# Kernel tuning notes

Hardware: AMD Instinct MI355X
Metric: run time of the kernel (lower is better)

The kernel has to match this reference:

```python
import jax, jax.numpy as jnp
import numpy as np

H = 256   # input_size
P = 256   # state_size
BATCH, L = 8, 4096
DT_MIN, DT_MAX = 1e-3, 1e-1
LN_EPS = 1e-5


def _hippo_params():
    # HiPPO-N matrix (num_blocks=1), eigendecomposition in numpy (float64 then cast)
    idx = np.arange(P, dtype=np.float64)
    s = np.sqrt(idx + 0.5)
    A = -np.outer(s, s)
    A = np.tril(A) - np.triu(A, 1)
    np.fill_diagonal(A, -0.5)
    ev, V = np.linalg.eig(A)
    order = np.argsort(ev.real)
    ev, V = ev[order], V[:, order]
    return ev, V


def setup_inputs() -> dict:
    key = jax.random.key(0)
    k_u, = jax.random.split(key, 1)
    ev, V = _hippo_params()
    rng = np.random.default_rng(0)
    log_lambda_real = np.log(-np.clip(ev.real, None, -1e-4)).astype(np.float32)
    lambda_imag = ev.imag.astype(np.float32)
    V_inv = np.linalg.inv(V)
    B_init = rng.standard_normal((P, H)) / np.sqrt(P)
    B_tilde = V_inv @ B_init.astype(np.complex128)
    C_init = rng.standard_normal((H, P)) / np.sqrt(P)
    C_tilde = C_init.astype(np.complex128) @ V
    log_delta = (rng.random(P) * (np.log(DT_MAX) - np.log(DT_MIN)) + np.log(DT_MIN)).astype(np.float32)
    return {
        "u": jax.random.normal(k_u, (BATCH, L, H), dtype=jnp.float32),
        "log_lambda_real": jnp.asarray(log_lambda_real),
        "lambda_imag": jnp.asarray(lambda_imag),
        "B_tilde_real": jnp.asarray(B_tilde.real, dtype=jnp.float32),
        "B_tilde_imag": jnp.asarray(B_tilde.imag, dtype=jnp.float32),
        "C_tilde_real": jnp.asarray(C_tilde.real, dtype=jnp.float32),
        "C_tilde_imag": jnp.asarray(C_tilde.imag, dtype=jnp.float32),
        "log_delta": jnp.asarray(log_delta),
        "gamma": jnp.ones((H,), dtype=jnp.float32),
        "beta": jnp.zeros((H,), dtype=jnp.float32),
    }


def _layernorm(x, gamma, beta):
    mu = jnp.mean(x, axis=-1, keepdims=True)
    var = jnp.mean(jnp.square(x - mu), axis=-1, keepdims=True)
    return (x - mu) * jax.lax.rsqrt(var + LN_EPS) * gamma + beta


def _ssm(h, log_lambda_real, lambda_imag, B_tilde_real, B_tilde_imag,
         C_tilde_real, C_tilde_imag, log_delta):
    # Continuous-time diagonal SSM params
    lam = -jnp.exp(log_lambda_real) + 1j * lambda_imag            # (P,) complex
    B_tilde = B_tilde_real + 1j * B_tilde_imag                     # (P,H)
    C_tilde = C_tilde_real + 1j * C_tilde_imag                     # (H,P)
    delta = jnp.exp(log_delta)                                     # (P,)
    # ZOH discretization (eq. 6 of the S5 paper)
    lambda_bar = jnp.exp(lam * delta)                              # (P,)
    B_bar = ((lambda_bar - 1.0) / lam)[:, None] * B_tilde          # (P,H)
    # Bu_k = B_bar @ u_k  ->  (B,L,P) complex
    Bu = jnp.einsum('blh,ph->blp', h.astype(jnp.complex64), B_bar.astype(jnp.complex64))
    # Parallel associative scan for x_k = lambda_bar * x_{k-1} + Bu_k
    a = jnp.broadcast_to(lambda_bar.astype(jnp.complex64), Bu.shape)
    def combine(c1, c2):
        a1, b1 = c1
        a2, b2 = c2
        return a1 * a2, a2 * b1 + b2
    _, xs = jax.lax.associative_scan(combine, (a, Bu), axis=1)     # (B,L,P)
    # Project back to real output: y = Re(C_tilde @ x)
    y = jnp.einsum('blp,hp->blh', xs, C_tilde.astype(jnp.complex64)).real
    return y


def reference(u, log_lambda_real, lambda_imag, B_tilde_real, B_tilde_imag,
              C_tilde_real, C_tilde_imag, log_delta, gamma, beta):
    # S5Block: pre-LayerNorm -> S5 SSM -> GELU -> residual
    h = _layernorm(u, gamma, beta)
    y = _ssm(h, log_lambda_real, lambda_imag, B_tilde_real, B_tilde_imag,
             C_tilde_real, C_tilde_imag, log_delta)
    return u + jax.nn.gelu(y)
```

## Files before the change

### kernel.cpp

```cpp
#include <hip/hip_runtime.h>
#include <math.h>

#define HDIM 256
#define PDIM 256
#define BATCH 8
#define LSEQ 4096
#define MTOT (BATCH * LSEQ)
#define CHLEN 128
#define NCHUNK 32

typedef __attribute__((ext_vector_type(8))) short bf16x8;
typedef __attribute__((ext_vector_type(4))) float f32x4;

__device__ __forceinline__ unsigned short f2bf(float f) {
    union { float f; unsigned int u; } v; v.f = f;
    unsigned int r = v.u + 0x7FFFu + ((v.u >> 16) & 1u);
    return (unsigned short)(r >> 16);
}
__device__ __forceinline__ float bf2f(unsigned int lo16) {
    union { unsigned int u; float f; } v; v.u = lo16 << 16;
    return v.f;
}

__global__ void params_k(const float* __restrict__ llr, const float* __restrict__ lim,
                         const float* __restrict__ ldl, float* __restrict__ par,
                         float* __restrict__ apw) {
    int p = threadIdx.x;
    float er = expf(llr[p]);
    float im = lim[p];
    float d  = expf(ldl[p]);
    float zr = -er * d, zi = im * d;
    float ea = expf(zr);
    float ar = ea * cosf(zi), ai = ea * sinf(zi);
    par[2 * p]     = ar;
    par[2 * p + 1] = ai;
    float pr = ar, pi = ai;
    apw[2 * p] = pr; apw[2 * p + 1] = pi;
    for (int j = 1; j < CHLEN; j++) {
        float nr = pr * ar - pi * ai;
        float ni = pr * ai + pi * ar;
        pr = nr; pi = ni;
        apw[j * 512 + 2 * p]     = pr;
        apw[j * 512 + 2 * p + 1] = pi;
    }
}

__global__ void w12_k(const float* __restrict__ Br, const float* __restrict__ Bi,
                      const float* __restrict__ Cr, const float* __restrict__ Ci,
                      const float* __restrict__ llr, const float* __restrict__ lim,
                      const float* __restrict__ ldl,
                      unsigned short* __restrict__ W1t, unsigned short* __restrict__ W2t) {
    int p = blockIdx.x, h = threadIdx.x;
    float er = expf(llr[p]);
    float im = lim[p];
    float d  = expf(ldl[p]);
    float zr = -er * d, zi = im * d;
    float ea = expf(zr);
    float ar = ea * cosf(zi), ai = ea * sinf(zi);
    float dr = -er, di = im;
    float den = dr * dr + di * di;
    float nr = ar - 1.0f, ni = ai;
    float cr = (nr * dr + ni * di) / den;
    float ci = (ni * dr - nr * di) / den;
    float br = Br[p * HDIM + h], bi = Bi[p * HDIM + h];
    W1t[(2 * p) * HDIM + h]     = f2bf(cr * br - ci * bi);
    W1t[(2 * p + 1) * HDIM + h] = f2bf(cr * bi + ci * br);
    W2t[h * 512 + 2 * p]     = f2bf(Cr[h * PDIM + p]);
    W2t[h * 512 + 2 * p + 1] = f2bf(-Ci[h * PDIM + p]);
}

__global__ void ln_k(const float* __restrict__ u, unsigned short* __restrict__ hbf,
                     const float* __restrict__ gamma, const float* __restrict__ beta) {
    __shared__ float gS[HDIM], bS[HDIM];
    int t = threadIdx.x;
    gS[t] = gamma[t]; bS[t] = beta[t];
    int lane = t & 63, wv = t >> 6;
    int row = blockIdx.x * 4 + wv;
    float4 v = *(const float4*)(u + (size_t)row * HDIM + lane * 4);
    float s  = v.x + v.y + v.z + v.w;
    float sq = v.x * v.x + v.y * v.y + v.z * v.z + v.w * v.w;
    #pragma unroll
    for (int o = 1; o < 64; o <<= 1) { s += __shfl_xor(s, o); sq += __shfl_xor(sq, o); }
    float mu = s * (1.0f / HDIM);
    float rs = rsqrtf(sq * (1.0f / HDIM) - mu * mu + 1e-5f);
    __syncthreads();
    int c = lane * 4;
    ushort4 o;
    o.x = f2bf((v.x - mu) * rs * gS[c + 0] + bS[c + 0]);
    o.y = f2bf((v.y - mu) * rs * gS[c + 1] + bS[c + 1]);
    o.z = f2bf((v.z - mu) * rs * gS[c + 2] + bS[c + 2]);
    o.w = f2bf((v.w - mu) * rs * gS[c + 3] + bS[c + 3]);
    *(ushort4*)(hbf + (size_t)row * HDIM + c) = o;
}

__launch_bounds__(256, 2)
__global__ void gemm1_k(const unsigned short* __restrict__ A, const unsigned short* __restrict__ B,
                        unsigned short* __restrict__ Bu, float* __restrict__ last,
                        const float* __restrict__ par, const float* __restrict__ apw) {
    __shared__ union {
        struct { unsigned short A[128 * 32]; unsigned short B[128 * 32]; } st;
        unsigned short C[128 * 128];
    } sm;

    const int t = threadIdx.x;
    const int bn = blockIdx.x, bm = blockIdx.y;
    const int lane = t & 63;
    const int wm = ((t >> 6) & 1) * 64;
    const int wn = ((t >> 6) >> 1) * 64;
    const int srow = t >> 1, skoff = (t & 1) * 16;
    const unsigned short* Ap = A + (size_t)(bm * 128 + srow) * 256 + skoff;
    const unsigned short* Bp = B + (size_t)(bn * 128 + srow) * 256 + skoff;
    const int mrow = lane & 15, kq = (lane >> 4) * 8;

    f32x4 acc[4][4] = {};

    for (int k0 = 0; k0 < 256; k0 += 32) {
        uint4 a0 = *(const uint4*)(Ap + k0);
        uint4 a1 = *(const uint4*)(Ap + k0 + 8);
        uint4 b0 = *(const uint4*)(Bp + k0);
        uint4 b1 = *(const uint4*)(Bp + k0 + 8);
        __syncthreads();
        *(uint4*)&sm.st.A[srow * 32 + skoff]     = a0;
        *(uint4*)&sm.st.A[srow * 32 + skoff + 8] = a1;
        *(uint4*)&sm.st.B[srow * 32 + skoff]     = b0;
        *(uint4*)&sm.st.B[srow * 32 + skoff + 8] = b1;
        __syncthreads();
        bf16x8 fa[4], fb[4];
        #pragma unroll
        for (int i = 0; i < 4; i++) {
            fa[i] = *(const bf16x8*)&sm.st.A[(wm + i * 16 + mrow) * 32 + kq];
            fb[i] = *(const bf16x8*)&sm.st.B[(wn + i * 16 + mrow) * 32 + kq];
        }
        #pragma unroll
        for (int i = 0; i < 4; i++)
            #pragma unroll
            for (int j = 0; j < 4; j++)
                acc[i][j] = __builtin_amdgcn_mfma_f32_16x16x32_bf16(fa[i], fb[j], acc[i][j], 0, 0, 0);
    }

    __syncthreads();
    const int r0 = (lane >> 4) * 4, c0 = lane & 15;
    #pragma unroll
    for (int i = 0; i < 4; i++)
        #pragma unroll
        for (int j = 0; j < 4; j++)
            #pragma unroll
            for (int r = 0; r < 4; r++)
                sm.C[(wm + i * 16 + r0 + r) * 128 + wn + j * 16 + c0] = f2bf(acc[i][j][r]);
    __syncthreads();

    if (t < 64) {
        int pg = bn * 64 + t;
        float ar = par[2 * pg], ai = par[2 * pg + 1];
        float xr = 0.0f, xi = 0.0f;
        unsigned int* Cw = (unsigned int*)sm.C;
        #pragma unroll 8
        for (int s = 0; s < CHLEN; s++) {
            unsigned int v = Cw[s * 64 + t];
            float vr = bf2f(v & 0xFFFFu), vi = bf2f(v >> 16);
            float nr = fmaf(ar, xr, fmaf(-ai, xi, vr));
            float ni = fmaf(ar, xi, fmaf(ai, xr, vi));
            xr = nr; xi = ni;
            Cw[s * 64 + t] = (unsigned int)f2bf(xr) | ((unsigned int)f2bf(xi) << 16);
        }
        *(float2*)(last + (size_t)(bm * 256 + pg) * 2) = make_float2(xr, xi);
    }
    __syncthreads();

    {
        int row = t >> 1, ch = (t & 1) * 64;
        unsigned short* dst = Bu + (size_t)(bm * 128 + row) * 512 + bn * 128 + ch;
        const unsigned short* src = &sm.C[row * 128 + ch];
        #pragma unroll
        for (int q = 0; q < 8; q++)
            *(uint4*)(dst + q * 8) = *(const uint4*)(src + q * 8);
    }
}

__global__ void carry_k(const float* __restrict__ last, float* __restrict__ prefix,
                        const float* __restrict__ apw) {
    int p = threadIdx.x, b = blockIdx.x;
    float Ar = apw[127 * 512 + 2 * p], Ai = apw[127 * 512 + 2 * p + 1];
    float Pr = 0.0f, Pi = 0.0f;
    for (int c = 0; c < NCHUNK; c++) {
        size_t idx = (size_t)((b * NCHUNK + c) * 256 + p) * 2;
        *(float2*)(prefix + idx) = make_float2(Pr, Pi);
        float2 l = *(const float2*)(last + idx);
        float nr = fmaf(Ar, Pr, fmaf(-Ai, Pi, l.x));
        float ni = fmaf(Ar, Pi, fmaf(Ai, Pr, l.y));
        Pr = nr; Pi = ni;
    }
}

__launch_bounds__(256, 2)
__global__ void gemm2_k(const unsigned short* __restrict__ Bu, const unsigned short* __restrict__ B,
                        float* __restrict__ out, const float* __restrict__ u,
                        const float* __restrict__ apw, const float* __restrict__ prefix) {
    __shared__ struct { unsigned short A[128 * 32]; unsigned short B[128 * 32]; } st;
    const int t = threadIdx.x;
    const int bn = blockIdx.x, bm = blockIdx.y;
    const int lane = t & 63;
    const int wm = ((t >> 6) & 1) * 64;
    const int wn = ((t >> 6) >> 1) * 64;
    const int srow = t >> 1, skoff = (t & 1) * 16;
    const unsigned short* Ap = Bu + (size_t)(bm * 128 + srow) * 512 + skoff;
    const unsigned short* Bp = B + (size_t)(bn * 128 + srow) * 512 + skoff;
    const float* fw = apw + srow * 512 + skoff;
    const float* pw = prefix + (size_t)bm * 512 + skoff;
    const int mrow = lane & 15, kq = (lane >> 4) * 8;

    f32x4 acc[4][4] = {};

    for (int k0 = 0; k0 < 512; k0 += 32) {
        uint4 q0 = *(const uint4*)(Ap + k0);
        uint4 q1 = *(const uint4*)(Ap + k0 + 8);
        uint4 b0 = *(const uint4*)(Bp + k0);
        uint4 b1 = *(const uint4*)(Bp + k0 + 8);
        float4 f0 = *(const float4*)(fw + k0),     f1 = *(const float4*)(fw + k0 + 4);
        float4 f2 = *(const float4*)(fw + k0 + 8), f3 = *(const float4*)(fw + k0 + 12);
        float4 g0 = *(const float4*)(pw + k0),     g1 = *(const float4*)(pw + k0 + 4);
        float4 g2 = *(const float4*)(pw + k0 + 8), g3 = *(const float4*)(pw + k0 + 12);
        __syncthreads();
        unsigned int qa[8] = {q0.x, q0.y, q0.z, q0.w, q1.x, q1.y, q1.z, q1.w};
        float fv[16], pv[16];
        *(float4*)&fv[0] = f0;  *(float4*)&fv[4] = f1;  *(float4*)&fv[8] = f2;  *(float4*)&fv[12] = f3;
        *(float4*)&pv[0] = g0;  *(float4*)&pv[4] = g1;  *(float4*)&pv[8] = g2;  *(float4*)&pv[12] = g3;
        unsigned int xo[8];
        #pragma unroll
        for (int e = 0; e < 8; e++) {
            float vr = bf2f(qa[e] & 0xFFFFu), vi = bf2f(qa[e] >> 16);
            float fr = fv[2 * e], fi = fv[2 * e + 1];
            float Pr = pv[2 * e], Pi = pv[2 * e + 1];
            float xr = fmaf(fr, Pr, fmaf(-fi, Pi, vr));
            float xi = fmaf(fr, Pi, fmaf(fi, Pr, vi));
            xo[e] = (unsigned int)f2bf(xr) | ((unsigned int)f2bf(xi) << 16);
        }
        *(uint4*)&st.A[srow * 32 + skoff]     = make_uint4(xo[0], xo[1], xo[2], xo[3]);
        *(uint4*)&st.A[srow * 32 + skoff + 8] = make_uint4(xo[4], xo[5], xo[6], xo[7]);
        *(uint4*)&st.B[srow * 32 + skoff]     = b0;
        *(uint4*)&st.B[srow * 32 + skoff + 8] = b1;
        __syncthreads();
        bf16x8 fa[4], fb[4];
        #pragma unroll
        for (int i = 0; i < 4; i++) {
            fa[i] = *(const bf16x8*)&st.A[(wm + i * 16 + mrow) * 32 + kq];
            fb[i] = *(const bf16x8*)&st.B[(wn + i * 16 + mrow) * 32 + kq];
        }
        #pragma unroll
        for (int i = 0; i < 4; i++)
            #pragma unroll
            for (int j = 0; j < 4; j++)
                acc[i][j] = __builtin_amdgcn_mfma_f32_16x16x32_bf16(fa[i], fb[j], acc[i][j], 0, 0, 0);
    }

    const int r0 = (lane >> 4) * 4, c0 = lane & 15;
    #pragma unroll
    for (int i = 0; i < 4; i++) {
        #pragma unroll
        for (int r = 0; r < 4; r++) {
            const size_t rowoff = (size_t)(bm * 128 + wm + i * 16 + r0 + r) * 256;
            #pragma unroll
            for (int j = 0; j < 4; j++) {
                const int col = bn * 128 + wn + j * 16 + c0;
                float y = acc[i][j][r];
                float z = 0.7978845608f * fmaf(0.044715f * y * y, y, y);
                float e = __expf(2.0f * z);
                float th = 1.0f - 2.0f / (e + 1.0f);
                float g = 0.5f * y * (1.0f + th);
                out[rowoff + col] = u[rowoff + col] + g;
            }
        }
    }
}

extern "C" void kernel_launch(void* const* d_in, const int* in_sizes, int n_in,
                              void* d_out, int out_size, void* d_ws, size_t ws_size,
                              hipStream_t stream) {
    const float* u   = (const float*)d_in[0];
    const float* llr = (const float*)d_in[1];
    const float* lim = (const float*)d_in[2];
    const float* Br  = (const float*)d_in[3];
    const float* Bi  = (const float*)d_in[4];
    const float* Cr  = (const float*)d_in[5];
    const float* Ci  = (const float*)d_in[6];
    const float* ldl = (const float*)d_in[7];
    const float* gam = (const float*)d_in[8];
    const float* bet = (const float*)d_in[9];
    float* out = (float*)d_out;

    float* ws     = (float*)d_ws;
    float* par    = ws;
    float* apw    = ws + 1024;
    float* last   = apw + 128 * 512;
    float* prefix = last + 256 * 256 * 2;
    unsigned short* W1t = (unsigned short*)(prefix + 256 * 256 * 2);
    unsigned short* W2t = W1t + 512 * HDIM;
    unsigned short* hbf = W2t + HDIM * 512;
    unsigned short* Bu  = hbf + (size_t)MTOT * HDIM;

    params_k<<<1, PDIM, 0, stream>>>(llr, lim, ldl, par, apw);
    w12_k<<<PDIM, HDIM, 0, stream>>>(Br, Bi, Cr, Ci, llr, lim, ldl, W1t, W2t);
    ln_k<<<MTOT / 4, 256, 0, stream>>>(u, hbf, gam, bet);

    gemm1_k<<<dim3(4, MTOT / 128), 256, 0, stream>>>(hbf, W1t, Bu, last, par, apw);

    carry_k<<<BATCH, PDIM, 0, stream>>>(last, prefix, apw);

    gemm2_k<<<dim3(2, MTOT / 128), 256, 0, stream>>>(Bu, W2t, out, u, apw, prefix);
}
```

Measured before the change: 184.6 us.

## Fuse LayerNorm, both GEMMs, chunk scan and carry into one persistent kernel

```diff
diff --git a/kernel.cpp b/kernel.cpp
--- a/kernel.cpp
+++ b/kernel.cpp
@@ -8,9 +8,11 @@
 #define MTOT (BATCH * LSEQ)
 #define CHLEN 128
 #define NCHUNK 32
+#define HSTR 264
 
 typedef __attribute__((ext_vector_type(8))) short bf16x8;
 typedef __attribute__((ext_vector_type(4))) float f32x4;
+typedef unsigned long long ull;
 
 __device__ __forceinline__ unsigned short f2bf(float f) {
     union { float f; unsigned int u; } v; v.f = f;
@@ -24,7 +26,7 @@
 
 __global__ void params_k(const float* __restrict__ llr, const float* __restrict__ lim,
                          const float* __restrict__ ldl, float* __restrict__ par,
-                         float* __restrict__ apw) {
+                         float* __restrict__ apw, float* __restrict__ Apow) {
     int p = threadIdx.x;
     float er = expf(llr[p]);
     float im = lim[p];
@@ -42,6 +44,16 @@
         pr = nr; pi = ni;
         apw[j * 512 + 2 * p]     = pr;
         apw[j * 512 + 2 * p + 1] = pi;
+    }
+    float A128r = pr, A128i = pi;
+    float cr = 1.0f, ci = 0.0f;
+    Apow[2 * p] = 1.0f; Apow[2 * p + 1] = 0.0f;
+    for (int m = 1; m < 32; m++) {
+        float nr = cr * A128r - ci * A128i;
+        float ni = cr * A128i + ci * A128r;
+        cr = nr; ci = ni;
+        Apow[m * 512 + 2 * p]     = cr;
+        Apow[m * 512 + 2 * p + 1] = ci;
     }
 }
 
@@ -69,205 +81,182 @@
     W2t[h * 512 + 2 * p + 1] = f2bf(-Ci[h * PDIM + p]);
 }
 
-__global__ void ln_k(const float* __restrict__ u, unsigned short* __restrict__ hbf,
-                     const float* __restrict__ gamma, const float* __restrict__ beta) {
-    __shared__ float gS[HDIM], bS[HDIM];
-    int t = threadIdx.x;
-    gS[t] = gamma[t]; bS[t] = beta[t];
-    int lane = t & 63, wv = t >> 6;
-    int row = blockIdx.x * 4 + wv;
-    float4 v = *(const float4*)(u + (size_t)row * HDIM + lane * 4);
-    float s  = v.x + v.y + v.z + v.w;
-    float sq = v.x * v.x + v.y * v.y + v.z * v.z + v.w * v.w;
-    #pragma unroll
-    for (int o = 1; o < 64; o <<= 1) { s += __shfl_xor(s, o); sq += __shfl_xor(sq, o); }
-    float mu = s * (1.0f / HDIM);
-    float rs = rsqrtf(sq * (1.0f / HDIM) - mu * mu + 1e-5f);
+__launch_bounds__(512, 1)
+__global__ void fused_k(const float* __restrict__ u,
+                        const unsigned short* __restrict__ W1t,
+                        const unsigned short* __restrict__ W2t,
+                        const float* __restrict__ par, const float* __restrict__ apw,
+                        const float* __restrict__ Apow,
+                        ull* __restrict__ Lbuf, int* __restrict__ flags,
+                        const float* __restrict__ gamma, const float* __restrict__ beta_p,
+                        float* __restrict__ out) {
+    __shared__ unsigned short hS[128 * HSTR];
+    __shared__ unsigned short BuS[128 * HSTR];
+    __shared__ float2 Pp[128];
+
+    const int t = threadIdx.x;
+    const int blk = blockIdx.x;
+    const int b = blk >> 5, c = blk & 31;
+    const int w = t >> 6, lane = t & 63;
+    const size_t rowbase = (size_t)blk * 128;
+
+    const int mrow = lane & 15, kq = (lane >> 4) * 8;
+    const int r0 = (lane >> 4) * 4, c0 = lane & 15;
+    const int wm1 = (w & 1) * 64, wn1 = (w >> 1) * 32;
+    const int wm2 = (w & 1) * 64, wn2 = (w >> 1) * 64;
+
+    {
+        const int cidx = lane * 4;
+        float4 g4 = *(const float4*)(gamma + cidx);
+        float4 b4 = *(const float4*)(beta_p + cidx);
+        const int rw = w * 16;
+        for (int it = 0; it < 16; ++it) {
+            int row = rw + it;
+            float4 v = *(const float4*)(u + (rowbase + row) * 256 + cidx);
+            float s  = v.x + v.y + v.z + v.w;
+            float sq = v.x * v.x + v.y * v.y + v.z * v.z + v.w * v.w;
+            #pragma unroll
+            for (int o = 1; o < 64; o <<= 1) { s += __shfl_xor(s, o); sq += __shfl_xor(sq, o); }
+            float mu = s * (1.0f / 256.0f);
+            float rs = rsqrtf(sq * (1.0f / 256.0f) - mu * mu + 1e-5f);
+            unsigned int w0 = (unsigned int)f2bf((v.x - mu) * rs * g4.x + b4.x)
+                            | ((unsigned int)f2bf((v.y - mu) * rs * g4.y + b4.y) << 16);
+            unsigned int w1 = (unsigned int)f2bf((v.z - mu) * rs * g4.z + b4.z)
+                            | ((unsigned int)f2bf((v.w - mu) * rs * g4.w + b4.w) << 16);
+            *(uint2*)&hS[row * HSTR + cidx] = make_uint2(w0, w1);
+        }
+    }
     __syncthreads();
-    int c = lane * 4;
-    ushort4 o;
-    o.x = f2bf((v.x - mu) * rs * gS[c + 0] + bS[c + 0]);
-    o.y = f2bf((v.y - mu) * rs * gS[c + 1] + bS[c + 1]);
-    o.z = f2bf((v.z - mu) * rs * gS[c + 2] + bS[c + 2]);
-    o.w = f2bf((v.w - mu) * rs * gS[c + 3] + bS[c + 3]);
-    *(ushort4*)(hbf + (size_t)row * HDIM + c) = o;
-}
-
-__launch_bounds__(256, 2)
-__global__ void gemm1_k(const unsigned short* __restrict__ A, const unsigned short* __restrict__ B,
-                        unsigned short* __restrict__ Bu, float* __restrict__ last,
-                        const float* __restrict__ par, const float* __restrict__ apw) {
-    __shared__ union {
-        struct { unsigned short A[128 * 32]; unsigned short B[128 * 32]; } st;
-        unsigned short C[128 * 128];
-    } sm;
-
-    const int t = threadIdx.x;
-    const int bn = blockIdx.x, bm = blockIdx.y;
-    const int lane = t & 63;
-    const int wm = ((t >> 6) & 1) * 64;
-    const int wn = ((t >> 6) >> 1) * 64;
-    const int srow = t >> 1, skoff = (t & 1) * 16;
-    const unsigned short* Ap = A + (size_t)(bm * 128 + srow) * 256 + skoff;
-    const unsigned short* Bp = B + (size_t)(bn * 128 + srow) * 256 + skoff;
-    const int mrow = lane & 15, kq = (lane >> 4) * 8;
-
-    f32x4 acc[4][4] = {};
-
-    for (int k0 = 0; k0 < 256; k0 += 32) {
-        uint4 a0 = *(const uint4*)(Ap + k0);
-        uint4 a1 = *(const uint4*)(Ap + k0 + 8);
-        uint4 b0 = *(const uint4*)(Bp + k0);
-        uint4 b1 = *(const uint4*)(Bp + k0 + 8);
-        __syncthreads();
-        *(uint4*)&sm.st.A[srow * 32 + skoff]     = a0;
-        *(uint4*)&sm.st.A[srow * 32 + skoff + 8] = a1;
-        *(uint4*)&sm.st.B[srow * 32 + skoff]     = b0;
-        *(uint4*)&sm.st.B[srow * 32 + skoff + 8] = b1;
-        __syncthreads();
-        bf16x8 fa[4], fb[4];
+
+    f32x4 acc2[4][4] = {};
+    unsigned int* BuW = (unsigned int*)BuS;
+
+    for (int half = 0; half < 2; ++half) {
+        __syncthreads();
+
         #pragma unroll
-        for (int i = 0; i < 4; i++) {
-            fa[i] = *(const bf16x8*)&sm.st.A[(wm + i * 16 + mrow) * 32 + kq];
-            fb[i] = *(const bf16x8*)&sm.st.B[(wn + i * 16 + mrow) * 32 + kq];
-        }
-        #pragma unroll
-        for (int i = 0; i < 4; i++)
-            #pragma unroll
-            for (int j = 0; j < 4; j++)
-                acc[i][j] = __builtin_amdgcn_mfma_f32_16x16x32_bf16(fa[i], fb[j], acc[i][j], 0, 0, 0);
-    }
-
-    __syncthreads();
-    const int r0 = (lane >> 4) * 4, c0 = lane & 15;
-    #pragma unroll
-    for (int i = 0; i < 4; i++)
-        #pragma unroll
-        for (int j = 0; j < 4; j++)
-            #pragma unroll
-            for (int r = 0; r < 4; r++)
-                sm.C[(wm + i * 16 + r0 + r) * 128 + wn + j * 16 + c0] = f2bf(acc[i][j][r]);
-    __syncthreads();
-
-    if (t < 64) {
-        int pg = bn * 64 + t;
-        float ar = par[2 * pg], ai = par[2 * pg + 1];
-        float xr = 0.0f, xi = 0.0f;
-        unsigned int* Cw = (unsigned int*)sm.C;
-        #pragma unroll 8
-        for (int s = 0; s < CHLEN; s++) {
-            unsigned int v = Cw[s * 64 + t];
-            float vr = bf2f(v & 0xFFFFu), vi = bf2f(v >> 16);
-            float nr = fmaf(ar, xr, fmaf(-ai, xi, vr));
-            float ni = fmaf(ar, xi, fmaf(ai, xr, vi));
-            xr = nr; xi = ni;
-            Cw[s * 64 + t] = (unsigned int)f2bf(xr) | ((unsigned int)f2bf(xi) << 16);
-        }
-        *(float2*)(last + (size_t)(bm * 256 + pg) * 2) = make_float2(xr, xi);
-    }
-    __syncthreads();
-
-    {
-        int row = t >> 1, ch = (t & 1) * 64;
-        unsigned short* dst = Bu + (size_t)(bm * 128 + row) * 512 + bn * 128 + ch;
-        const unsigned short* src = &sm.C[row * 128 + ch];
-        #pragma unroll
-        for (int q = 0; q < 8; q++)
-            *(uint4*)(dst + q * 8) = *(const uint4*)(src + q * 8);
-    }
-}
-
-__global__ void carry_k(const float* __restrict__ last, float* __restrict__ prefix,
-                        const float* __restrict__ apw) {
-    int p = threadIdx.x, b = blockIdx.x;
-    float Ar = apw[127 * 512 + 2 * p], Ai = apw[127 * 512 + 2 * p + 1];
-    float Pr = 0.0f, Pi = 0.0f;
-    for (int c = 0; c < NCHUNK; c++) {
-        size_t idx = (size_t)((b * NCHUNK + c) * 256 + p) * 2;
-        *(float2*)(prefix + idx) = make_float2(Pr, Pi);
-        float2 l = *(const float2*)(last + idx);
-        float nr = fmaf(Ar, Pr, fmaf(-Ai, Pi, l.x));
-        float ni = fmaf(Ar, Pi, fmaf(Ai, Pr, l.y));
-        Pr = nr; Pi = ni;
-    }
-}
-
-__launch_bounds__(256, 2)
-__global__ void gemm2_k(const unsigned short* __restrict__ Bu, const unsigned short* __restrict__ B,
-                        float* __restrict__ out, const float* __restrict__ u,
-                        const float* __restrict__ apw, const float* __restrict__ prefix) {
-    __shared__ struct { unsigned short A[128 * 32]; unsigned short B[128 * 32]; } st;
-    const int t = threadIdx.x;
-    const int bn = blockIdx.x, bm = blockIdx.y;
-    const int lane = t & 63;
-    const int wm = ((t >> 6) & 1) * 64;
-    const int wn = ((t >> 6) >> 1) * 64;
-    const int srow = t >> 1, skoff = (t & 1) * 16;
-    const unsigned short* Ap = Bu + (size_t)(bm * 128 + srow) * 512 + skoff;
-    const unsigned short* Bp = B + (size_t)(bn * 128 + srow) * 512 + skoff;
-    const float* fw = apw + srow * 512 + skoff;
-    const float* pw = prefix + (size_t)bm * 512 + skoff;
-    const int mrow = lane & 15, kq = (lane >> 4) * 8;
-
-    f32x4 acc[4][4] = {};
-
-    for (int k0 = 0; k0 < 512; k0 += 32) {
-        uint4 q0 = *(const uint4*)(Ap + k0);
-        uint4 q1 = *(const uint4*)(Ap + k0 + 8);
-        uint4 b0 = *(const uint4*)(Bp + k0);
-        uint4 b1 = *(const uint4*)(Bp + k0 + 8);
-        float4 f0 = *(const float4*)(fw + k0),     f1 = *(const float4*)(fw + k0 + 4);
-        float4 f2 = *(const float4*)(fw + k0 + 8), f3 = *(const float4*)(fw + k0 + 12);
-        float4 g0 = *(const float4*)(pw + k0),     g1 = *(const float4*)(pw + k0 + 4);
-        float4 g2 = *(const float4*)(pw + k0 + 8), g3 = *(const float4*)(pw + k0 + 12);
-        __syncthreads();
-        unsigned int qa[8] = {q0.x, q0.y, q0.z, q0.w, q1.x, q1.y, q1.z, q1.w};
-        float fv[16], pv[16];
-        *(float4*)&fv[0] = f0;  *(float4*)&fv[4] = f1;  *(float4*)&fv[8] = f2;  *(float4*)&fv[12] = f3;
-        *(float4*)&pv[0] = g0;  *(float4*)&pv[4] = g1;  *(float4*)&pv[8] = g2;  *(float4*)&pv[12] = g3;
-        unsigned int xo[8];
-        #pragma unroll
-        for (int e = 0; e < 8; e++) {
-            float vr = bf2f(qa[e] & 0xFFFFu), vi = bf2f(qa[e] >> 16);
-            float fr = fv[2 * e], fi = fv[2 * e + 1];
-            float Pr = pv[2 * e], Pi = pv[2 * e + 1];
-            float xr = fmaf(fr, Pr, fmaf(-fi, Pi, vr));
-            float xi = fmaf(fr, Pi, fmaf(fi, Pr, vi));
-            xo[e] = (unsigned int)f2bf(xr) | ((unsigned int)f2bf(xi) << 16);
-        }
-        *(uint4*)&st.A[srow * 32 + skoff]     = make_uint4(xo[0], xo[1], xo[2], xo[3]);
-        *(uint4*)&st.A[srow * 32 + skoff + 8] = make_uint4(xo[4], xo[5], xo[6], xo[7]);
-        *(uint4*)&st.B[srow * 32 + skoff]     = b0;
-        *(uint4*)&st.B[srow * 32 + skoff + 8] = b1;
-        __syncthreads();
-        bf16x8 fa[4], fb[4];
-        #pragma unroll
-        for (int i = 0; i < 4; i++) {
-            fa[i] = *(const bf16x8*)&st.A[(wm + i * 16 + mrow) * 32 + kq];
-            fb[i] = *(const bf16x8*)&st.B[(wn + i * 16 + mrow) * 32 + kq];
-        }
-        #pragma unroll
-        for (int i = 0; i < 4; i++)
-            #pragma unroll
-            for (int j = 0; j < 4; j++)
-                acc[i][j] = __builtin_amdgcn_mfma_f32_16x16x32_bf16(fa[i], fb[j], acc[i][j], 0, 0, 0);
-    }
-
-    const int r0 = (lane >> 4) * 4, c0 = lane & 15;
+        for (int ncl = 0; ncl < 2; ++ncl) {
+            const int nc = half * 2 + ncl;
+            f32x4 acc1[4][2] = {};
+            const unsigned short* Wb = W1t + (size_t)(nc * 128 + wn1 + mrow) * 256 + kq;
+            #pragma unroll
+            for (int ks = 0; ks < 8; ++ks) {
+                const int k0 = ks * 32;
+                bf16x8 fb0 = *(const bf16x8*)(Wb + k0);
+                bf16x8 fb1 = *(const bf16x8*)(Wb + 16 * 256 + k0);
+                bf16x8 fa[4];
+                #pragma unroll
+                for (int i = 0; i < 4; i++)
+                    fa[i] = *(const bf16x8*)&hS[(wm1 + i * 16 + mrow) * HSTR + k0 + kq];
+                #pragma unroll
+                for (int i = 0; i < 4; i++) {
+                    acc1[i][0] = __builtin_amdgcn_mfma_f32_16x16x32_bf16(fa[i], fb0, acc1[i][0], 0, 0, 0);
+                    acc1[i][1] = __builtin_amdgcn_mfma_f32_16x16x32_bf16(fa[i], fb1, acc1[i][1], 0, 0, 0);
+                }
+            }
+            #pragma unroll
+            for (int i = 0; i < 4; i++)
+                #pragma unroll
+                for (int j = 0; j < 2; j++)
+                    #pragma unroll
+                    for (int r = 0; r < 4; r++)
+                        BuS[(wm1 + i * 16 + r0 + r) * HSTR + ncl * 128 + wn1 + j * 16 + c0]
+                            = f2bf(acc1[i][j][r]);
+        }
+        __syncthreads();
+
+        if (t < 128) {
+            const int pg = half * 128 + t;
+            float ar = par[2 * pg], ai = par[2 * pg + 1];
+            float xr = 0.0f, xi = 0.0f;
+            #pragma unroll 8
+            for (int j = 0; j < 128; j++) {
+                unsigned int v = BuW[j * (HSTR / 2) + t];
+                float vr = bf2f(v & 0xFFFFu), vi = bf2f(v >> 16);
+                float nr = fmaf(ar, xr, fmaf(-ai, xi, vr));
+                float ni = fmaf(ar, xi, fmaf(ai, xr, vi));
+                xr = nr; xi = ni;
+                BuW[j * (HSTR / 2) + t] = (unsigned int)f2bf(xr) | ((unsigned int)f2bf(xi) << 16);
+            }
+            union { float f[2]; ull u; } pk; pk.f[0] = xr; pk.f[1] = xi;
+            __hip_atomic_store(&Lbuf[(size_t)(half * 256 + blk) * 128 + t], pk.u,
+                               __ATOMIC_RELAXED, __HIP_MEMORY_SCOPE_AGENT);
+        }
+        __syncthreads();
+        if (t == 0)
+            __hip_atomic_store(&flags[half * 256 + blk], 1,
+                               __ATOMIC_RELEASE, __HIP_MEMORY_SCOPE_AGENT);
+
+        if (t < 128) {
+            const int pg = half * 128 + t;
+            float Pr = 0.0f, Pi = 0.0f;
+            for (int k = 0; k < c; ++k) {
+                const int fi = half * 256 + b * 32 + k;
+                while (__hip_atomic_load(&flags[fi], __ATOMIC_ACQUIRE,
+                                         __HIP_MEMORY_SCOPE_AGENT) == 0) {}
+                union { float f[2]; ull u; } lk;
+                lk.u = __hip_atomic_load(&Lbuf[(size_t)fi * 128 + t],
+                                         __ATOMIC_RELAXED, __HIP_MEMORY_SCOPE_AGENT);
+                const float2 Am = *(const float2*)(Apow + (size_t)(c - 1 - k) * 512 + 2 * pg);
+                Pr = fmaf(Am.x, lk.f[0], fmaf(-Am.y, lk.f[1], Pr));
+                Pi = fmaf(Am.x, lk.f[1], fmaf(Am.y, lk.f[0], Pi));
+            }
+            Pp[t] = make_float2(Pr, Pi);
+        }
+        __syncthreads();
+
+        if (c > 0) {
+            const int j = t >> 2, cs = (t & 3) * 32;
+            const float2* ap = (const float2*)apw + (size_t)j * 256 + half * 128 + cs;
+            #pragma unroll 8
+            for (int i = 0; i < 32; i++) {
+                float2 a2 = ap[i];
+                float2 P  = Pp[cs + i];
+                unsigned int v = BuW[j * (HSTR / 2) + cs + i];
+                float vr = bf2f(v & 0xFFFFu), vi = bf2f(v >> 16);
+                float xr = fmaf(a2.x, P.x, fmaf(-a2.y, P.y, vr));
+                float xi = fmaf(a2.x, P.y, fmaf(a2.y, P.x, vi));
+                BuW[j * (HSTR / 2) + cs + i] = (unsigned int)f2bf(xr) | ((unsigned int)f2bf(xi) << 16);
+            }
+        }
+        __syncthreads();
+
+        {
+            const unsigned short* Wb = W2t + (size_t)(wn2 + mrow) * 512 + half * 256 + kq;
+            #pragma unroll
+            for (int ks = 0; ks < 8; ++ks) {
+                const int k0 = ks * 32;
+                bf16x8 fb[4];
+                #pragma unroll
+                for (int j = 0; j < 4; j++)
+                    fb[j] = *(const bf16x8*)(Wb + (size_t)j * 16 * 512 + k0);
+                bf16x8 fa[4];
+                #pragma unroll
+                for (int i = 0; i < 4; i++)
+                    fa[i] = *(const bf16x8*)&BuS[(wm2 + i * 16 + mrow) * HSTR + k0 + kq];
+                #pragma unroll
+                for (int i = 0; i < 4; i++)
+                    #pragma unroll
+                    for (int j = 0; j < 4; j++)
+                        acc2[i][j] = __builtin_amdgcn_mfma_f32_16x16x32_bf16(fa[i], fb[j], acc2[i][j], 0, 0, 0);
+            }
+        }
+    }
+
     #pragma unroll
     for (int i = 0; i < 4; i++) {
         #pragma unroll
         for (int r = 0; r < 4; r++) {
-            const size_t rowoff = (size_t)(bm * 128 + wm + i * 16 + r0 + r) * 256;
+            const size_t gr = rowbase + wm2 + i * 16 + r0 + r;
+            const float* up = u + gr * 256 + wn2 + c0;
+            float* op = out + gr * 256 + wn2 + c0;
             #pragma unroll
             for (int j = 0; j < 4; j++) {
-                const int col = bn * 128 + wn + j * 16 + c0;
-                float y = acc[i][j][r];
+                float y = acc2[i][j][r];
                 float z = 0.7978845608f * fmaf(0.044715f * y * y, y, y);
                 float e = __expf(2.0f * z);
                 float th = 1.0f - 2.0f / (e + 1.0f);
-                float g = 0.5f * y * (1.0f + th);
-                out[rowoff + col] = u[rowoff + col] + g;
+                op[j * 16] = up[j * 16] + 0.5f * y * (1.0f + th);
             }
         }
     }
@@ -288,23 +277,19 @@
     const float* bet = (const float*)d_in[9];
     float* out = (float*)d_out;
 
-    float* ws     = (float*)d_ws;
-    float* par    = ws;
-    float* apw    = ws + 1024;
-    float* last   = apw + 128 * 512;
-    float* prefix = last + 256 * 256 * 2;
-    unsigned short* W1t = (unsigned short*)(prefix + 256 * 256 * 2);
-    unsigned short* W2t = W1t + 512 * HDIM;
-    unsigned short* hbf = W2t + HDIM * 512;
-    unsigned short* Bu  = hbf + (size_t)MTOT * HDIM;
-
-    params_k<<<1, PDIM, 0, stream>>>(llr, lim, ldl, par, apw);
+    char* ws = (char*)d_ws;
+    float* par   = (float*)(ws);
+    float* apw   = (float*)(ws + 2048);
+    float* Apow  = (float*)(ws + 266240);
+    int*   flags = (int*)  (ws + 331776);
+    ull*   Lbuf  = (ull*)  (ws + 335872);
+    unsigned short* W1t = (unsigned short*)(ws + 860160);
+    unsigned short* W2t = (unsigned short*)(ws + 1122304);
+
+    hipMemsetAsync(flags, 0, 2 * 256 * sizeof(int), stream);
+    params_k<<<1, PDIM, 0, stream>>>(llr, lim, ldl, par, apw, Apow);
     w12_k<<<PDIM, HDIM, 0, stream>>>(Br, Bi, Cr, Ci, llr, lim, ldl, W1t, W2t);
-    ln_k<<<MTOT / 4, 256, 0, stream>>>(u, hbf, gam, bet);
-
-    gemm1_k<<<dim3(4, MTOT / 128), 256, 0, stream>>>(hbf, W1t, Bu, last, par, apw);
-
-    carry_k<<<BATCH, PDIM, 0, stream>>>(last, prefix, apw);
-
-    gemm2_k<<<dim3(2, MTOT / 128), 256, 0, stream>>>(Bu, W2t, out, u, apw, prefix);
-}
+
+    fused_k<<<BATCH * NCHUNK, 512, 0, stream>>>(u, W1t, W2t, par, apw, Apow,
+                                                Lbuf, flags, gam, bet, out);
+}
```

New measurement: 313.9 us. 1.7x slower.

## Split carry application into separate pass and merge param kernels

Applied to the files above, without the earlier changes.

```diff
diff --git a/kernel.cpp b/kernel.cpp
--- a/kernel.cpp
+++ b/kernel.cpp
@@ -22,34 +22,12 @@
     return v.f;
 }
 
-__global__ void params_k(const float* __restrict__ llr, const float* __restrict__ lim,
-                         const float* __restrict__ ldl, float* __restrict__ par,
-                         float* __restrict__ apw) {
-    int p = threadIdx.x;
-    float er = expf(llr[p]);
-    float im = lim[p];
-    float d  = expf(ldl[p]);
-    float zr = -er * d, zi = im * d;
-    float ea = expf(zr);
-    float ar = ea * cosf(zi), ai = ea * sinf(zi);
-    par[2 * p]     = ar;
-    par[2 * p + 1] = ai;
-    float pr = ar, pi = ai;
-    apw[2 * p] = pr; apw[2 * p + 1] = pi;
-    for (int j = 1; j < CHLEN; j++) {
-        float nr = pr * ar - pi * ai;
-        float ni = pr * ai + pi * ar;
-        pr = nr; pi = ni;
-        apw[j * 512 + 2 * p]     = pr;
-        apw[j * 512 + 2 * p + 1] = pi;
-    }
-}
-
-__global__ void w12_k(const float* __restrict__ Br, const float* __restrict__ Bi,
-                      const float* __restrict__ Cr, const float* __restrict__ Ci,
-                      const float* __restrict__ llr, const float* __restrict__ lim,
-                      const float* __restrict__ ldl,
-                      unsigned short* __restrict__ W1t, unsigned short* __restrict__ W2t) {
+__global__ void prep_k(const float* __restrict__ Br, const float* __restrict__ Bi,
+                       const float* __restrict__ Cr, const float* __restrict__ Ci,
+                       const float* __restrict__ llr, const float* __restrict__ lim,
+                       const float* __restrict__ ldl,
+                       unsigned short* __restrict__ W1t, unsigned short* __restrict__ W2t,
+                       float* __restrict__ par, float* __restrict__ apw) {
     int p = blockIdx.x, h = threadIdx.x;
     float er = expf(llr[p]);
     float im = lim[p];
@@ -67,6 +45,19 @@
     W1t[(2 * p + 1) * HDIM + h] = f2bf(cr * bi + ci * br);
     W2t[h * 512 + 2 * p]     = f2bf(Cr[h * PDIM + p]);
     W2t[h * 512 + 2 * p + 1] = f2bf(-Ci[h * PDIM + p]);
+    if (h == 0) {
+        par[2 * p]     = ar;
+        par[2 * p + 1] = ai;
+        float pr = ar, pi = ai;
+        apw[2 * p] = pr; apw[2 * p + 1] = pi;
+        for (int j = 1; j < CHLEN; j++) {
+            float tr = pr * ar - pi * ai;
+            float ti = pr * ai + pi * ar;
+            pr = tr; pi = ti;
+            apw[j * 512 + 2 * p]     = pr;
+            apw[j * 512 + 2 * p + 1] = pi;
+        }
+    }
 }
 
 __global__ void ln_k(const float* __restrict__ u, unsigned short* __restrict__ hbf,
@@ -192,59 +183,64 @@
     }
 }
 
+__global__ void apply_k(unsigned short* __restrict__ Bu, const float* __restrict__ apw,
+                        const float* __restrict__ prefix) {
+    int c = blockIdx.x;
+    if (c == 0) return;
+    int b = blockIdx.y;
+    int t = threadIdx.x;
+    int k = t & 255;
+    int j0 = (t >> 8) * 64;
+    float2 P = *(const float2*)(prefix + ((size_t)(b * NCHUNK + c) * 256 + k) * 2);
+    unsigned int* q = (unsigned int*)(Bu + ((size_t)b * LSEQ + (size_t)c * CHLEN + j0) * 512) + k;
+    const float2* ap = (const float2*)apw + (size_t)j0 * 256 + k;
+    #pragma unroll 4
+    for (int j = 0; j < 64; j++) {
+        float2 a2 = ap[(size_t)j * 256];
+        unsigned int v = q[(size_t)j * 256];
+        float vr = bf2f(v & 0xFFFFu), vi = bf2f(v >> 16);
+        float xr = fmaf(a2.x, P.x, fmaf(-a2.y, P.y, vr));
+        float xi = fmaf(a2.x, P.y, fmaf(a2.y, P.x, vi));
+        q[(size_t)j * 256] = (unsigned int)f2bf(xr) | ((unsigned int)f2bf(xi) << 16);
+    }
+}
+
+#define LDK 40
 __launch_bounds__(256, 2)
-__global__ void gemm2_k(const unsigned short* __restrict__ Bu, const unsigned short* __restrict__ B,
-                        float* __restrict__ out, const float* __restrict__ u,
-                        const float* __restrict__ apw, const float* __restrict__ prefix) {
-    __shared__ struct { unsigned short A[128 * 32]; unsigned short B[128 * 32]; } st;
+__global__ void gemm2_k(const unsigned short* __restrict__ A, const unsigned short* __restrict__ B,
+                        float* __restrict__ out, const float* __restrict__ u) {
+    __shared__ unsigned short As[128 * LDK];
+    __shared__ unsigned short Bs[128 * LDK];
     const int t = threadIdx.x;
     const int bn = blockIdx.x, bm = blockIdx.y;
     const int lane = t & 63;
     const int wm = ((t >> 6) & 1) * 64;
     const int wn = ((t >> 6) >> 1) * 64;
     const int srow = t >> 1, skoff = (t & 1) * 16;
-    const unsigned short* Ap = Bu + (size_t)(bm * 128 + srow) * 512 + skoff;
+    const unsigned short* Ap = A + (size_t)(bm * 128 + srow) * 512 + skoff;
     const unsigned short* Bp = B + (size_t)(bn * 128 + srow) * 512 + skoff;
-    const float* fw = apw + srow * 512 + skoff;
-    const float* pw = prefix + (size_t)bm * 512 + skoff;
+    unsigned short* AsW = &As[srow * LDK + skoff];
+    unsigned short* BsW = &Bs[srow * LDK + skoff];
     const int mrow = lane & 15, kq = (lane >> 4) * 8;
 
     f32x4 acc[4][4] = {};
 
     for (int k0 = 0; k0 < 512; k0 += 32) {
-        uint4 q0 = *(const uint4*)(Ap + k0);
-        uint4 q1 = *(const uint4*)(Ap + k0 + 8);
+        uint4 a0 = *(const uint4*)(Ap + k0);
+        uint4 a1 = *(const uint4*)(Ap + k0 + 8);
         uint4 b0 = *(const uint4*)(Bp + k0);
         uint4 b1 = *(const uint4*)(Bp + k0 + 8);
-        float4 f0 = *(const float4*)(fw + k0),     f1 = *(const float4*)(fw + k0 + 4);
-        float4 f2 = *(const float4*)(fw + k0 + 8), f3 = *(const float4*)(fw + k0 + 12);
-        float4 g0 = *(const float4*)(pw + k0),     g1 = *(const float4*)(pw + k0 + 4);
-        float4 g2 = *(const float4*)(pw + k0 + 8), g3 = *(const float4*)(pw + k0 + 12);
         __syncthreads();
-        unsigned int qa[8] = {q0.x, q0.y, q0.z, q0.w, q1.x, q1.y, q1.z, q1.w};
-        float fv[16], pv[16];
-        *(float4*)&fv[0] = f0;  *(float4*)&fv[4] = f1;  *(float4*)&fv[8] = f2;  *(float4*)&fv[12] = f3;
-        *(float4*)&pv[0] = g0;  *(float4*)&pv[4] = g1;  *(float4*)&pv[8] = g2;  *(float4*)&pv[12] = g3;
-        unsigned int xo[8];
-        #pragma unroll
-        for (int e = 0; e < 8; e++) {
-            float vr = bf2f(qa[e] & 0xFFFFu), vi = bf2f(qa[e] >> 16);
-            float fr = fv[2 * e], fi = fv[2 * e + 1];
-            float Pr = pv[2 * e], Pi = pv[2 * e + 1];
-            float xr = fmaf(fr, Pr, fmaf(-fi, Pi, vr));
-            float xi = fmaf(fr, Pi, fmaf(fi, Pr, vi));
-            xo[e] = (unsigned int)f2bf(xr) | ((unsigned int)f2bf(xi) << 16);
-        }
-        *(uint4*)&st.A[srow * 32 + skoff]     = make_uint4(xo[0], xo[1], xo[2], xo[3]);
-        *(uint4*)&st.A[srow * 32 + skoff + 8] = make_uint4(xo[4], xo[5], xo[6], xo[7]);
-        *(uint4*)&st.B[srow * 32 + skoff]     = b0;
-        *(uint4*)&st.B[srow * 32 + skoff + 8] = b1;
+        *(uint4*)AsW       = a0;
+        *(uint4*)(AsW + 8) = a1;
+        *(uint4*)BsW       = b0;
+        *(uint4*)(BsW + 8) = b1;
         __syncthreads();
         bf16x8 fa[4], fb[4];
         #pragma unroll
         for (int i = 0; i < 4; i++) {
-            fa[i] = *(const bf16x8*)&st.A[(wm + i * 16 + mrow) * 32 + kq];
-            fb[i] = *(const bf16x8*)&st.B[(wn + i * 16 + mrow) * 32 + kq];
+            fa[i] = *(const bf16x8*)&As[(wm + i * 16 + mrow) * LDK + kq];
+            fb[i] = *(const bf16x8*)&Bs[(wn + i * 16 + mrow) * LDK + kq];
         }
         #pragma unroll
         for (int i = 0; i < 4; i++)
@@ -266,8 +262,7 @@
                 float z = 0.7978845608f * fmaf(0.044715f * y * y, y, y);
                 float e = __expf(2.0f * z);
                 float th = 1.0f - 2.0f / (e + 1.0f);
-                float g = 0.5f * y * (1.0f + th);
-                out[rowoff + col] = u[rowoff + col] + g;
+                out[rowoff + col] = u[rowoff + col] + 0.5f * y * (1.0f + th);
             }
         }
     }
@@ -298,13 +293,14 @@
     unsigned short* hbf = W2t + HDIM * 512;
     unsigned short* Bu  = hbf + (size_t)MTOT * HDIM;
 
-    params_k<<<1, PDIM, 0, stream>>>(llr, lim, ldl, par, apw);
-    w12_k<<<PDIM, HDIM, 0, stream>>>(Br, Bi, Cr, Ci, llr, lim, ldl, W1t, W2t);
+    prep_k<<<PDIM, HDIM, 0, stream>>>(Br, Bi, Cr, Ci, llr, lim, ldl, W1t, W2t, par, apw);
     ln_k<<<MTOT / 4, 256, 0, stream>>>(u, hbf, gam, bet);
 
     gemm1_k<<<dim3(4, MTOT / 128), 256, 0, stream>>>(hbf, W1t, Bu, last, par, apw);
 
     carry_k<<<BATCH, PDIM, 0, stream>>>(last, prefix, apw);
 
-    gemm2_k<<<dim3(2, MTOT / 128), 256, 0, stream>>>(Bu, W2t, out, u, apw, prefix);
-}
+    apply_k<<<dim3(NCHUNK, BATCH), 512, 0, stream>>>(Bu, apw, prefix);
+
+    gemm2_k<<<dim3(2, MTOT / 128), 256, 0, stream>>>(Bu, W2t, out, u);
+}
```

Result: faster. 177.4 us (-3.9%).
